# Kernel tuning notes

Hardware: AMD Instinct MI355X
Metric: run time of the kernel (lower is better)

## Reference

```python
import jax, jax.numpy as jnp
import numpy as np
import math

B, T, C, NH = 4, 2048, 1024, 16
D = C // NH  # 64, rotary_dim == D

def _rope_tables():
    inv_freq = 1.0 / (10000.0 ** (np.arange(0, D, 2, dtype=np.float32) / D))
    t = np.arange(T, dtype=np.float32)
    freqs = np.outer(t, inv_freq)                 # [T, D/2]
    emb = np.concatenate([freqs, freqs], axis=-1)  # [T, D]
    return jnp.asarray(np.cos(emb))[None], jnp.asarray(np.sin(emb))[None]  # [1,T,D]

def setup_inputs() -> dict:
    key = jax.random.key(0)
    ks = jax.random.split(key, 3)
    x = jax.random.normal(ks[0], (B, T, C), dtype=jnp.float32)
    w_attn = jax.random.normal(ks[1], (3 * C, C), dtype=jnp.float32) * (1.0 / math.sqrt(C))
    b_attn = jnp.zeros((3 * C,), dtype=jnp.float32)
    w_proj = jax.random.normal(ks[2], (C, C), dtype=jnp.float32) * (1.0 / math.sqrt(C))
    b_proj = jnp.zeros((C,), dtype=jnp.float32)
    cos, sin = _rope_tables()
    return {"x": x, "w_attn": w_attn, "b_attn": b_attn,
            "w_proj": w_proj, "b_proj": b_proj, "cos": cos, "sin": sin}

def _rotate_half(u):
    u1, u2 = jnp.split(u, 2, axis=-1)
    return jnp.concatenate([-u2, u1], axis=-1)

def reference(x, w_attn, b_attn, w_proj, b_proj, cos, sin):
    Bx, Tx, Cx = x.shape
    nh, d = NH, Cx // NH
    # fused QKV projection (torch Linear: y = x @ W^T + b)
    qkv = x @ w_attn.T + b_attn                      # [B,T,3C]
    q, k, v = jnp.split(qkv, 3, axis=-1)
    q = q.reshape(Bx, Tx, nh, d).transpose(0, 2, 1, 3)  # [B,nh,T,d]
    k = k.reshape(Bx, Tx, nh, d).transpose(0, 2, 1, 3)
    v = v.reshape(Bx, Tx, nh, d).transpose(0, 2, 1, 3)
    # RoPE (rotary_dim == d, full head)
    c = cos[:, None, :, :]  # [1,1,T,d]
    s = sin[:, None, :, :]
    q = q * c + _rotate_half(q) * s
    k = k * c + _rotate_half(k) * s
    # naive causal attention
    scores = jnp.einsum("bhqd,bhkd->bhqk", q, k) / math.sqrt(d)
    causal = jnp.tril(jnp.ones((Tx, Tx), dtype=bool))
    scores = jnp.where(causal[None, None], scores, -jnp.inf)
    att = jax.nn.softmax(scores, axis=-1)
    y = jnp.einsum("bhqk,bhkd->bhqd", att, v)        # [B,nh,T,d]
    y = y.transpose(0, 2, 1, 3).reshape(Bx, Tx, Cx)
    return y @ w_proj.T + b_proj
```

## Files before the change

### kernel.cpp

```cpp
#include <hip/hip_runtime.h>

typedef __bf16 bf16_t;
typedef bf16_t bf16x8 __attribute__((ext_vector_type(8)));
typedef bf16_t bf16x4 __attribute__((ext_vector_type(4)));
typedef float f32x4 __attribute__((ext_vector_type(4)));

constexpr int BATCH = 4, SEQ = 2048, CH = 1024, NHEAD = 16, HD = 64;
constexpr int BM = 128, BN = 128, BKK = 64;

#define LGKM_FENCE() __asm__ __volatile__("s_waitcnt lgkmcnt(0)" ::: "memory")
#define VM_FENCE() __asm__ __volatile__("s_waitcnt vmcnt(0)" ::: "memory")

__device__ __forceinline__ void g2lds16(const bf16_t* g, bf16_t* l) {
  __builtin_amdgcn_global_load_lds((__attribute__((address_space(1))) void*)(g),
                                   (__attribute__((address_space(3))) void*)(l),
                                   16, 0, 0);
}

__device__ __forceinline__ f32x4 mfma16(bf16x8 a, bf16x8 b, f32x4 c) {
  return __builtin_amdgcn_mfma_f32_16x16x32_bf16(a, b, c, 0, 0, 0);
}

__global__ __launch_bounds__(256) void cvt3_kernel(const float4* __restrict__ x,
                                                   ushort4* __restrict__ dx,
                                                   const float4* __restrict__ wa,
                                                   ushort4* __restrict__ dwa,
                                                   const float4* __restrict__ wp,
                                                   ushort4* __restrict__ dwp) {
  int bid = blockIdx.x;
  const float4* s;
  ushort4* d;
  int i;
  if (bid < 8192) {
    s = x; d = dx; i = bid * 256 + threadIdx.x;
  } else if (bid < 11264) {
    s = wa; d = dwa; i = (bid - 8192) * 256 + threadIdx.x;
  } else {
    s = wp; d = dwp; i = (bid - 11264) * 256 + threadIdx.x;
  }
  float4 f = s[i];
  ushort4 o;
  o.x = __builtin_bit_cast(unsigned short, (bf16_t)f.x);
  o.y = __builtin_bit_cast(unsigned short, (bf16_t)f.y);
  o.z = __builtin_bit_cast(unsigned short, (bf16_t)f.z);
  o.w = __builtin_bit_cast(unsigned short, (bf16_t)f.w);
  d[i] = o;
}

__device__ __forceinline__ void gemm_mainloop(const bf16_t* __restrict__ A,
                                              const bf16_t* __restrict__ W, int Kdim,
                                              int m0, int n0,
                                              bf16_t* As, bf16_t* Bs,
                                              f32x4 acc[4][4]) {
  const int tid = threadIdx.x;
  const int lane = tid & 63;
  const int w = tid >> 6;
  const int quad = lane >> 4, l16 = lane & 15;
  const int wm = (w >> 1) << 6, wn = (w & 1) << 6;
  const int srow = tid >> 3;
  const int scol = ((tid & 7) ^ (srow & 7)) << 3;
  const int dcol = (tid & 7) << 3;
  const int key = l16 & 15 & 7;
  const bf16_t* ga[4];
  const bf16_t* gb[4];
  bf16_t *la[4], *lb[4];
#pragma unroll
  for (int p = 0; p < 4; p++) {
    int row = p * 32 + srow;
    ga[p] = A + (size_t)(m0 + row) * Kdim + scol;
    gb[p] = W + (size_t)(n0 + row) * Kdim + scol;
    la[p] = As + row * BKK + dcol;
    lb[p] = Bs + row * BKK + dcol;
  }
  for (int k0 = 0; k0 < Kdim; k0 += BKK) {
#pragma unroll
    for (int p = 0; p < 4; p++) g2lds16(ga[p] + k0, la[p]);
#pragma unroll
    for (int p = 0; p < 4; p++) g2lds16(gb[p] + k0, lb[p]);
    VM_FENCE();
    __syncthreads();
#pragma unroll
    for (int ki = 0; ki < 2; ki++) {
      bf16x8 av[4], bv[4];
#pragma unroll
      for (int i = 0; i < 4; i++)
        av[i] = *(const bf16x8*)&As[(wm + i * 16 + l16) * BKK +
                                    ((((ki << 2) | quad) ^ key) << 3)];
#pragma unroll
      for (int i = 0; i < 4; i++)
        bv[i] = *(const bf16x8*)&Bs[(wn + i * 16 + l16) * BKK +
                                    ((((ki << 2) | quad) ^ key) << 3)];
#pragma unroll
      for (int mi = 0; mi < 4; mi++)
#pragma unroll
        for (int ni = 0; ni < 4; ni++)
          acc[mi][ni] = mfma16(av[mi], bv[ni], acc[mi][ni]);
    }
    __syncthreads();
  }
}

constexpr float SCL = 0.125f * 1.44269504089f;

__global__ __launch_bounds__(256) void qkv_rope_kernel(
    const bf16_t* __restrict__ X, const bf16_t* __restrict__ Wa,
    const float* __restrict__ ba, const float* __restrict__ cosT,
    const float* __restrict__ sinT, bf16_t* __restrict__ Q,
    bf16_t* __restrict__ Ko, bf16_t* __restrict__ VT) {
  constexpr int TSTRIDE = 68;
  __shared__ __align__(16) char smem[4 * 64 * TSTRIDE * 2];
  bf16_t* As = (bf16_t*)smem;
  bf16_t* Bs = As + BM * BKK;

  f32x4 acc[4][4];
#pragma unroll
  for (int i = 0; i < 4; i++)
#pragma unroll
    for (int j = 0; j < 4; j++) acc[i][j] = (f32x4){0.f, 0.f, 0.f, 0.f};

  const int id = blockIdx.x;
  const int sid = ((id & 7) * 192) + (id >> 3);
  const int n0 = (sid % 24) * BN;
  const int m0 = (sid / 24) * BM;
  gemm_mainloop(X, Wa, CH, m0, n0, As, Bs, acc);

  const int tid = threadIdx.x, lane = tid & 63, w = tid >> 6;
  const int quad = lane >> 4, l16 = lane & 15;
  const int wm = (w >> 1) << 6, wn = (w & 1) << 6;
  const int nbase = n0 + wn;
  const int part = nbase >> 10;
  const int h = (nbase & 1023) >> 6;
  const int mbase = m0 + wm;
  const int bb = mbase >> 11;
  const size_t headbase = ((size_t)(bb * NHEAD + h)) * SEQ * HD;

  if (part < 2) {
    bf16_t* O = (part == 0) ? Q : Ko;
    const float post = (part == 0) ? SCL : 1.0f;
#pragma unroll
    for (int mi = 0; mi < 4; mi++)
#pragma unroll
      for (int r = 0; r < 4; r++) {
        int m = mbase + mi * 16 + quad * 4 + r;
        int t = m & (SEQ - 1);
        const float* cr = cosT + t * HD;
        const float* sr = sinT + t * HD;
        size_t rowo = headbase + (size_t)t * HD;
#pragma unroll
        for (int ni = 0; ni < 2; ni++) {
          int d0 = ni * 16 + l16, d1 = d0 + 32;
          float v0 = acc[mi][ni][r] + ba[nbase + d0];
          float v1 = acc[mi][ni + 2][r] + ba[nbase + d1];
          float r0 = (v0 * cr[d0] - v1 * sr[d0]) * post;
          float r1 = (v1 * cr[d1] + v0 * sr[d1]) * post;
          O[rowo + d0] = (bf16_t)r0;
          O[rowo + d1] = (bf16_t)r1;
        }
      }
  } else {
    bf16_t* tb = (bf16_t*)smem + w * 64 * TSTRIDE;
    int t0 = mbase & (SEQ - 1);
#pragma unroll
    for (int mi = 0; mi < 4; mi++)
#pragma unroll
      for (int ni = 0; ni < 4; ni++) {
        int d = ni * 16 + l16;
        float bias = ba[nbase + d];
#pragma unroll
        for (int r = 0; r < 4; r++) {
          float v = acc[mi][ni][r] + bias;
          tb[d * TSTRIDE + mi * 16 + quad * 4 + r] = (bf16_t)v;
        }
      }
    LGKM_FENCE();
    int half = lane >> 5, l5 = lane & 31;
    size_t vbase = ((size_t)(bb * NHEAD + h)) * HD * SEQ;
#pragma unroll
    for (int it = 0; it < 32; it++) {
      int d = it * 2 + half;
      unsigned int val = *(const unsigned int*)&tb[d * TSTRIDE + l5 * 2];
      *(unsigned int*)&VT[vbase + (size_t)d * SEQ + t0 + l5 * 2] = val;
    }
  }
}

__device__ __forceinline__ void sm_update(f32x4 (&s)[4], float& lr,
                                          bf16_t* Prow, int quad,
                                          int swz, bool domask, int lim) {
  if (domask) {
#pragma unroll
    for (int ni = 0; ni < 4; ni++)
#pragma unroll
      for (int r = 0; r < 4; r++)
        if (ni * 16 + r > lim) s[ni][r] = -1e30f;
  }
  float sum = 0.f;
#pragma unroll
  for (int ni = 0; ni < 4; ni++) {
    float p0 = __builtin_exp2f(s[ni][0]);
    float p1 = __builtin_exp2f(s[ni][1]);
    float p2 = __builtin_exp2f(s[ni][2]);
    float p3 = __builtin_exp2f(s[ni][3]);
    bf16x4 pk = {(bf16_t)p0, (bf16_t)p1, (bf16_t)p2, (bf16_t)p3};
    *(bf16x4*)&Prow[(((ni << 2) | quad) ^ (swz << 1)) << 2] = pk;
    sum += (p0 + p1) + (p2 + p3);
  }
  lr += sum;
}

__global__ __launch_bounds__(256) void flash_kernel(const bf16_t* __restrict__ Q,
                                                    const bf16_t* __restrict__ Kg,
                                                    const bf16_t* __restrict__ VT,
                                                    bf16_t* __restrict__ att) {
  __shared__ __align__(16) bf16_t Ks[2][64 * 64];
  __shared__ __align__(16) bf16_t Vs[2][64 * 64];
  __shared__ __align__(16) bf16_t Pt[4][16 * 64];
  const int tid = threadIdx.x, w = tid >> 6, lane = tid & 63;
  const int quad = lane >> 4, l16 = lane & 15;
  const int p = (int)blockIdx.x >> 6;
  const int bh = (int)blockIdx.x & 63;
  const bf16_t* Qp = Q + (size_t)bh * SEQ * HD;
  const bf16_t* Kb = Kg + (size_t)bh * SEQ * HD;
  const bf16_t* Vb = VT + (size_t)bh * HD * SEQ;
  const int grow = lane >> 3;
  const int gj8 = ((lane & 7) ^ grow) * 8;
  const int i0 = w * 2;
  const int sw = l16 & 7;
  const int swz = l16 >> 1;
  const int bloc = bh >> 4, hh = bh & 15;
  bf16_t* Pw = &Pt[w][l16 * 64];
  const int rs0 = (quad ^ swz) << 3;
  const int rs1 = ((4 + quad) ^ swz) << 3;

  auto stage = [&](int kcs, int b) {
#pragma unroll
    for (int ii = 0; ii < 2; ii++) {
      int i = i0 + ii;
      g2lds16(Kb + (size_t)(kcs + i * 8 + grow) * HD + gj8, &Ks[b][(i * 64 + lane) * 8]);
      g2lds16(Vb + (size_t)(i * 8 + grow) * SEQ + kcs + gj8, &Vs[b][(i * 64 + lane) * 8]);
    }
  };

  for (int sp = 0; sp < 2; ++sp) {
    const int j = sp ? p : 31 - p;
    const int m = j * 64 + w * 16;
    const int nch = j + 1;
    bf16x8 aq0 = *(const bf16x8*)&Qp[(size_t)(m + l16) * HD + quad * 8];
    bf16x8 aq1 = *(const bf16x8*)&Qp[(size_t)(m + l16) * HD + 32 + quad * 8];
    float lr = 0.f;
    f32x4 y[4];
#pragma unroll
    for (int ni = 0; ni < 4; ni++) y[ni] = (f32x4){0.f, 0.f, 0.f, 0.f};

    stage(0, 0);
    VM_FENCE();
    __syncthreads();

    for (int c = 0; c < nch; ++c) {
      const int kc = c * 64, buf = c & 1;
      if (c + 1 < nch) stage(kc + 64, buf ^ 1);
      f32x4 s[4];
#pragma unroll
      for (int ni = 0; ni < 4; ni++) {
        bf16x8 k0 = *(const bf16x8*)&Ks[buf][((ni * 16 + l16) * 8 + (quad ^ sw)) * 8];
        bf16x8 k1 = *(const bf16x8*)&Ks[buf][((ni * 16 + l16) * 8 + ((4 + quad) ^ sw)) * 8];
        f32x4 z = (f32x4){0.f, 0.f, 0.f, 0.f};
        s[ni] = mfma16(k1, aq1, mfma16(k0, aq0, z));
      }
      sm_update(s, lr, Pw, quad, swz, c == nch - 1, m + l16 - kc - quad * 4);
      LGKM_FENCE();
      bf16x8 p0 = *(const bf16x8*)&Pw[rs0];
      bf16x8 p1 = *(const bf16x8*)&Pw[rs1];
#pragma unroll
      for (int ni = 0; ni < 4; ni++) {
        bf16x8 v0 = *(const bf16x8*)&Vs[buf][((ni * 16 + l16) * 8 + (quad ^ sw)) * 8];
        bf16x8 v1 = *(const bf16x8*)&Vs[buf][((ni * 16 + l16) * 8 + ((4 + quad) ^ sw)) * 8];
        y[ni] = mfma16(v1, p1, mfma16(v0, p0, y[ni]));
      }
      VM_FENCE();
      __syncthreads();
    }

    lr += __shfl_xor(lr, 16);
    lr += __shfl_xor(lr, 32);
    float inv = 1.f / lr;
    size_t rb = ((size_t)bloc * SEQ + m + l16) * CH + hh * HD + quad * 4;
#pragma unroll
    for (int ni = 0; ni < 4; ni++) {
      bf16x4 o = {(bf16_t)(y[ni][0] * inv), (bf16_t)(y[ni][1] * inv),
                  (bf16_t)(y[ni][2] * inv), (bf16_t)(y[ni][3] * inv)};
      *(bf16x4*)&att[rb + ni * 16] = o;
    }
  }
}

__global__ __launch_bounds__(256) void proj_kernel(const bf16_t* __restrict__ A,
                                                   const bf16_t* __restrict__ Wp,
                                                   const float* __restrict__ bp,
                                                   float* __restrict__ out) {
  __shared__ __align__(16) bf16_t As[BM * BKK];
  __shared__ __align__(16) bf16_t Bs[BN * BKK];
  f32x4 acc[4][4];
#pragma unroll
  for (int i = 0; i < 4; i++)
#pragma unroll
    for (int j = 0; j < 4; j++) acc[i][j] = (f32x4){0.f, 0.f, 0.f, 0.f};
  const int id = blockIdx.x;
  const int sid = ((id & 7) * 64) + (id >> 3);
  const int n0 = (sid % 8) * BN;
  const int m0 = (sid / 8) * BM;
  gemm_mainloop(A, Wp, CH, m0, n0, As, Bs, acc);
  const int tid = threadIdx.x, lane = tid & 63, w = tid >> 6;
  const int quad = lane >> 4, l16 = lane & 15;
  const int wm = (w >> 1) << 6, wn = (w & 1) << 6;
  const int nbase = n0 + wn, mbase = m0 + wm;
#pragma unroll
  for (int mi = 0; mi < 4; mi++)
#pragma unroll
    for (int r = 0; r < 4; r++) {
      int m = mbase + mi * 16 + quad * 4 + r;
#pragma unroll
      for (int ni = 0; ni < 4; ni++) {
        int n = nbase + ni * 16 + l16;
        out[(size_t)m * CH + n] = acc[mi][ni][r] + bp[n];
      }
    }
}

extern "C" void kernel_launch(void* const* d_in, const int* in_sizes, int n_in,
                              void* d_out, int out_size, void* d_ws, size_t ws_size,
                              hipStream_t stream) {
  const float* x      = (const float*)d_in[0];
  const float* w_attn = (const float*)d_in[1];
  const float* b_attn = (const float*)d_in[2];
  const float* w_proj = (const float*)d_in[3];
  const float* b_proj = (const float*)d_in[4];
  const float* cosT   = (const float*)d_in[5];
  const float* sinT   = (const float*)d_in[6];
  float* out = (float*)d_out;

  bf16_t* xbf  = (bf16_t*)d_ws;
  bf16_t* wabf = xbf + (size_t)8192 * 1024;
  bf16_t* wpbf = wabf + (size_t)3072 * 1024;
  bf16_t* Qb   = wpbf + (size_t)1024 * 1024;
  bf16_t* Kb   = Qb + (size_t)8388608;
  bf16_t* VTb  = Kb + (size_t)8388608;
  bf16_t* attb = VTb + (size_t)8388608;

  cvt3_kernel<<<12288, 256, 0, stream>>>((const float4*)x, (ushort4*)xbf,
                                         (const float4*)w_attn, (ushort4*)wabf,
                                         (const float4*)w_proj, (ushort4*)wpbf);
  qkv_rope_kernel<<<dim3(1536), 256, 0, stream>>>(xbf, wabf, b_attn, cosT, sinT,
                                                  Qb, Kb, VTb);
  flash_kernel<<<dim3(1024), 256, 0, stream>>>(Qb, Kb, VTb, attb);
  proj_kernel<<<dim3(512), 256, 0, stream>>>(attb, wpbf, b_proj, out);
}
```

Measured before the change: 266.8 us.

## Process two 64-row query tiles per warp group to reuse staged K/V chunks

Each flash attention block now handles a 128-row query block by giving every wave two 16-row query tiles, so each staged K/V chunk in LDS feeds twice as many MFMAs. The grid is halved to 512 blocks, with the two query tiles paired causally (15-p and p) to balance load. The P scratch buffer is doubled per wave. The cost is higher register pressure and fewer blocks in flight, which may reduce occupancy and hide latency less well.

After: 267.4 us. Within noise of the previous version (+0.2%).

```diff
diff --git a/kernel.cpp b/kernel.cpp
--- a/kernel.cpp
+++ b/kernel.cpp
@@ -60,7 +60,7 @@
   const int srow = tid >> 3;
   const int scol = ((tid & 7) ^ (srow & 7)) << 3;
   const int dcol = (tid & 7) << 3;
-  const int key = l16 & 15 & 7;
+  const int key = l16 & 7;
   const bf16_t* ga[4];
   const bf16_t* gb[4];
   bf16_t *la[4], *lb[4];
@@ -214,7 +214,7 @@
                                                     bf16_t* __restrict__ att) {
   __shared__ __align__(16) bf16_t Ks[2][64 * 64];
   __shared__ __align__(16) bf16_t Vs[2][64 * 64];
-  __shared__ __align__(16) bf16_t Pt[4][16 * 64];
+  __shared__ __align__(16) bf16_t Pt[4][2][16 * 64];
   const int tid = threadIdx.x, w = tid >> 6, lane = tid & 63;
   const int quad = lane >> 4, l16 = lane & 15;
   const int p = (int)blockIdx.x >> 6;
@@ -228,7 +228,8 @@
   const int sw = l16 & 7;
   const int swz = l16 >> 1;
   const int bloc = bh >> 4, hh = bh & 15;
-  bf16_t* Pw = &Pt[w][l16 * 64];
+  bf16_t* Pw0 = &Pt[w][0][l16 * 64];
+  bf16_t* Pw1 = &Pt[w][1][l16 * 64];
   const int rs0 = (quad ^ swz) << 3;
   const int rs1 = ((4 + quad) ^ swz) << 3;
 
@@ -242,15 +243,22 @@
   };
 
   for (int sp = 0; sp < 2; ++sp) {
-    const int j = sp ? p : 31 - p;
-    const int m = j * 64 + w * 16;
-    const int nch = j + 1;
-    bf16x8 aq0 = *(const bf16x8*)&Qp[(size_t)(m + l16) * HD + quad * 8];
-    bf16x8 aq1 = *(const bf16x8*)&Qp[(size_t)(m + l16) * HD + 32 + quad * 8];
-    float lr = 0.f;
-    f32x4 y[4];
-#pragma unroll
-    for (int ni = 0; ni < 4; ni++) y[ni] = (f32x4){0.f, 0.f, 0.f, 0.f};
+    const int jb = sp ? p : 15 - p;
+    const int mb = jb * 128;
+    const int m0t = mb + w * 16;
+    const int m1t = mb + 64 + w * 16;
+    const int nch = 2 * jb + 2;
+    bf16x8 aq00 = *(const bf16x8*)&Qp[(size_t)(m0t + l16) * HD + quad * 8];
+    bf16x8 aq01 = *(const bf16x8*)&Qp[(size_t)(m0t + l16) * HD + 32 + quad * 8];
+    bf16x8 aq10 = *(const bf16x8*)&Qp[(size_t)(m1t + l16) * HD + quad * 8];
+    bf16x8 aq11 = *(const bf16x8*)&Qp[(size_t)(m1t + l16) * HD + 32 + quad * 8];
+    float lr0 = 0.f, lr1 = 0.f;
+    f32x4 y0[4], y1[4];
+#pragma unroll
+    for (int ni = 0; ni < 4; ni++) {
+      y0[ni] = (f32x4){0.f, 0.f, 0.f, 0.f};
+      y1[ni] = (f32x4){0.f, 0.f, 0.f, 0.f};
+    }
 
     stage(0, 0);
     VM_FENCE();
@@ -259,37 +267,63 @@
     for (int c = 0; c < nch; ++c) {
       const int kc = c * 64, buf = c & 1;
       if (c + 1 < nch) stage(kc + 64, buf ^ 1);
-      f32x4 s[4];
-#pragma unroll
-      for (int ni = 0; ni < 4; ni++) {
-        bf16x8 k0 = *(const bf16x8*)&Ks[buf][((ni * 16 + l16) * 8 + (quad ^ sw)) * 8];
-        bf16x8 k1 = *(const bf16x8*)&Ks[buf][((ni * 16 + l16) * 8 + ((4 + quad) ^ sw)) * 8];
+      const bool do0 = (c + 1 < nch);
+      bf16x8 kf[8];
+#pragma unroll
+      for (int ni = 0; ni < 4; ni++) {
+        kf[2 * ni]     = *(const bf16x8*)&Ks[buf][((ni * 16 + l16) * 8 + (quad ^ sw)) * 8];
+        kf[2 * ni + 1] = *(const bf16x8*)&Ks[buf][((ni * 16 + l16) * 8 + ((4 + quad) ^ sw)) * 8];
+      }
+      f32x4 s0[4], s1[4];
+#pragma unroll
+      for (int ni = 0; ni < 4; ni++) {
         f32x4 z = (f32x4){0.f, 0.f, 0.f, 0.f};
-        s[ni] = mfma16(k1, aq1, mfma16(k0, aq0, z));
-      }
-      sm_update(s, lr, Pw, quad, swz, c == nch - 1, m + l16 - kc - quad * 4);
+        s1[ni] = mfma16(kf[2 * ni + 1], aq11, mfma16(kf[2 * ni], aq10, z));
+      }
+      if (do0) {
+#pragma unroll
+        for (int ni = 0; ni < 4; ni++) {
+          f32x4 z = (f32x4){0.f, 0.f, 0.f, 0.f};
+          s0[ni] = mfma16(kf[2 * ni + 1], aq01, mfma16(kf[2 * ni], aq00, z));
+        }
+      }
+      sm_update(s1, lr1, Pw1, quad, swz, c == nch - 1, m1t + l16 - kc - quad * 4);
+      if (do0)
+        sm_update(s0, lr0, Pw0, quad, swz, c == nch - 2, m0t + l16 - kc - quad * 4);
       LGKM_FENCE();
-      bf16x8 p0 = *(const bf16x8*)&Pw[rs0];
-      bf16x8 p1 = *(const bf16x8*)&Pw[rs1];
+      bf16x8 p10 = *(const bf16x8*)&Pw1[rs0];
+      bf16x8 p11 = *(const bf16x8*)&Pw1[rs1];
+      bf16x8 p00, p01;
+      if (do0) {
+        p00 = *(const bf16x8*)&Pw0[rs0];
+        p01 = *(const bf16x8*)&Pw0[rs1];
+      }
 #pragma unroll
       for (int ni = 0; ni < 4; ni++) {
         bf16x8 v0 = *(const bf16x8*)&Vs[buf][((ni * 16 + l16) * 8 + (quad ^ sw)) * 8];
         bf16x8 v1 = *(const bf16x8*)&Vs[buf][((ni * 16 + l16) * 8 + ((4 + quad) ^ sw)) * 8];
-        y[ni] = mfma16(v1, p1, mfma16(v0, p0, y[ni]));
+        y1[ni] = mfma16(v1, p11, mfma16(v0, p10, y1[ni]));
+        if (do0) y0[ni] = mfma16(v1, p01, mfma16(v0, p00, y0[ni]));
       }
       VM_FENCE();
       __syncthreads();
     }
 
-    lr += __shfl_xor(lr, 16);
-    lr += __shfl_xor(lr, 32);
-    float inv = 1.f / lr;
-    size_t rb = ((size_t)bloc * SEQ + m + l16) * CH + hh * HD + quad * 4;
+    lr0 += __shfl_xor(lr0, 16);
+    lr0 += __shfl_xor(lr0, 32);
+    lr1 += __shfl_xor(lr1, 16);
+    lr1 += __shfl_xor(lr1, 32);
+    float inv0 = 1.f / lr0, inv1 = 1.f / lr1;
+    size_t rb0 = ((size_t)bloc * SEQ + m0t + l16) * CH + hh * HD + quad * 4;
+    size_t rb1 = ((size_t)bloc * SEQ + m1t + l16) * CH + hh * HD + quad * 4;
 #pragma unroll
     for (int ni = 0; ni < 4; ni++) {
-      bf16x4 o = {(bf16_t)(y[ni][0] * inv), (bf16_t)(y[ni][1] * inv),
-                  (bf16_t)(y[ni][2] * inv), (bf16_t)(y[ni][3] * inv)};
-      *(bf16x4*)&att[rb + ni * 16] = o;
+      bf16x4 o0 = {(bf16_t)(y0[ni][0] * inv0), (bf16_t)(y0[ni][1] * inv0),
+                   (bf16_t)(y0[ni][2] * inv0), (bf16_t)(y0[ni][3] * inv0)};
+      bf16x4 o1 = {(bf16_t)(y1[ni][0] * inv1), (bf16_t)(y1[ni][1] * inv1),
+                   (bf16_t)(y1[ni][2] * inv1), (bf16_t)(y1[ni][3] * inv1)};
+      *(bf16x4*)&att[rb0 + ni * 16] = o0;
+      *(bf16x4*)&att[rb1 + ni * 16] = o1;
     }
   }
 }
@@ -352,6 +386,6 @@
                                          (const float4*)w_proj, (ushort4*)wpbf);
   qkv_rope_kernel<<<dim3(1536), 256, 0, stream>>>(xbf, wabf, b_attn, cosT, sinT,
                                                   Qb, Kb, VTb);
-  flash_kernel<<<dim3(1024), 256, 0, stream>>>(Qb, Kb, VTb, attb);
+  flash_kernel<<<dim3(512), 256, 0, stream>>>(Qb, Kb, VTb, attb);
   proj_kernel<<<dim3(512), 256, 0, stream>>>(attb, wpbf, b_proj, out);
 }
```

## Process paired high/low query tiles in one KV sweep sharing staged K/V

Applied to the files above, without the earlier changes.

Instead of two sequential passes (one for the high query tile, one for the low), the attention block streams K/V once and applies each chunk to both query tiles, with the low tile active only for its first chunks. This removes the second staging pass over K/V for the low tile and shares K fragments loaded from LDS between the two tiles. It also adds s_setprio around the MFMA sections to favour matrix issue. The cost is higher register pressure from two accumulator sets and extra Q fragments. The Pw scratch buffer is reused serially by both tiles within an iteration.

Measured after the change: 274.0 us. 1.03x slower.

```diff
diff --git a/kernel.cpp b/kernel.cpp
--- a/kernel.cpp
+++ b/kernel.cpp
@@ -60,7 +60,7 @@
   const int srow = tid >> 3;
   const int scol = ((tid & 7) ^ (srow & 7)) << 3;
   const int dcol = (tid & 7) << 3;
-  const int key = l16 & 15 & 7;
+  const int key = l16 & 7;
   const bf16_t* ga[4];
   const bf16_t* gb[4];
   bf16_t *la[4], *lb[4];
@@ -241,56 +241,100 @@
     }
   };
 
-  for (int sp = 0; sp < 2; ++sp) {
-    const int j = sp ? p : 31 - p;
-    const int m = j * 64 + w * 16;
-    const int nch = j + 1;
-    bf16x8 aq0 = *(const bf16x8*)&Qp[(size_t)(m + l16) * HD + quad * 8];
-    bf16x8 aq1 = *(const bf16x8*)&Qp[(size_t)(m + l16) * HD + 32 + quad * 8];
-    float lr = 0.f;
-    f32x4 y[4];
-#pragma unroll
-    for (int ni = 0; ni < 4; ni++) y[ni] = (f32x4){0.f, 0.f, 0.f, 0.f};
-
-    stage(0, 0);
-    VM_FENCE();
-    __syncthreads();
-
-    for (int c = 0; c < nch; ++c) {
-      const int kc = c * 64, buf = c & 1;
-      if (c + 1 < nch) stage(kc + 64, buf ^ 1);
+  const int jh = 31 - p, jl = p;
+  const int mh = jh * 64 + w * 16;
+  const int ml = jl * 64 + w * 16;
+  const int nch_h = 32 - p;
+  const int nch_l = p + 1;
+
+  bf16x8 aqh0 = *(const bf16x8*)&Qp[(size_t)(mh + l16) * HD + quad * 8];
+  bf16x8 aqh1 = *(const bf16x8*)&Qp[(size_t)(mh + l16) * HD + 32 + quad * 8];
+  bf16x8 aql0 = *(const bf16x8*)&Qp[(size_t)(ml + l16) * HD + quad * 8];
+  bf16x8 aql1 = *(const bf16x8*)&Qp[(size_t)(ml + l16) * HD + 32 + quad * 8];
+  float lrh = 0.f, lrl = 0.f;
+  f32x4 yh[4], yl[4];
+#pragma unroll
+  for (int ni = 0; ni < 4; ni++) {
+    yh[ni] = (f32x4){0.f, 0.f, 0.f, 0.f};
+    yl[ni] = (f32x4){0.f, 0.f, 0.f, 0.f};
+  }
+
+  stage(0, 0);
+  VM_FENCE();
+  __syncthreads();
+
+  for (int c = 0; c < nch_h; ++c) {
+    const int kc = c * 64, buf = c & 1;
+    if (c + 1 < nch_h) stage(kc + 64, buf ^ 1);
+    bf16x8 kf[8];
+#pragma unroll
+    for (int ni = 0; ni < 4; ni++) {
+      kf[2 * ni]     = *(const bf16x8*)&Ks[buf][((ni * 16 + l16) * 8 + (quad ^ sw)) * 8];
+      kf[2 * ni + 1] = *(const bf16x8*)&Ks[buf][((ni * 16 + l16) * 8 + ((4 + quad) ^ sw)) * 8];
+    }
+    {
       f32x4 s[4];
-#pragma unroll
-      for (int ni = 0; ni < 4; ni++) {
-        bf16x8 k0 = *(const bf16x8*)&Ks[buf][((ni * 16 + l16) * 8 + (quad ^ sw)) * 8];
-        bf16x8 k1 = *(const bf16x8*)&Ks[buf][((ni * 16 + l16) * 8 + ((4 + quad) ^ sw)) * 8];
+      __builtin_amdgcn_s_setprio(1);
+#pragma unroll
+      for (int ni = 0; ni < 4; ni++) {
         f32x4 z = (f32x4){0.f, 0.f, 0.f, 0.f};
-        s[ni] = mfma16(k1, aq1, mfma16(k0, aq0, z));
-      }
-      sm_update(s, lr, Pw, quad, swz, c == nch - 1, m + l16 - kc - quad * 4);
+        s[ni] = mfma16(kf[2 * ni + 1], aqh1, mfma16(kf[2 * ni], aqh0, z));
+      }
+      __builtin_amdgcn_s_setprio(0);
+      sm_update(s, lrh, Pw, quad, swz, c == nch_h - 1, mh + l16 - kc - quad * 4);
       LGKM_FENCE();
       bf16x8 p0 = *(const bf16x8*)&Pw[rs0];
       bf16x8 p1 = *(const bf16x8*)&Pw[rs1];
+      __builtin_amdgcn_s_setprio(1);
 #pragma unroll
       for (int ni = 0; ni < 4; ni++) {
         bf16x8 v0 = *(const bf16x8*)&Vs[buf][((ni * 16 + l16) * 8 + (quad ^ sw)) * 8];
         bf16x8 v1 = *(const bf16x8*)&Vs[buf][((ni * 16 + l16) * 8 + ((4 + quad) ^ sw)) * 8];
-        y[ni] = mfma16(v1, p1, mfma16(v0, p0, y[ni]));
-      }
-      VM_FENCE();
-      __syncthreads();
-    }
-
-    lr += __shfl_xor(lr, 16);
-    lr += __shfl_xor(lr, 32);
-    float inv = 1.f / lr;
-    size_t rb = ((size_t)bloc * SEQ + m + l16) * CH + hh * HD + quad * 4;
-#pragma unroll
-    for (int ni = 0; ni < 4; ni++) {
-      bf16x4 o = {(bf16_t)(y[ni][0] * inv), (bf16_t)(y[ni][1] * inv),
-                  (bf16_t)(y[ni][2] * inv), (bf16_t)(y[ni][3] * inv)};
-      *(bf16x4*)&att[rb + ni * 16] = o;
-    }
+        yh[ni] = mfma16(v1, p1, mfma16(v0, p0, yh[ni]));
+      }
+      __builtin_amdgcn_s_setprio(0);
+    }
+    if (c < nch_l) {
+      f32x4 s[4];
+      __builtin_amdgcn_s_setprio(1);
+#pragma unroll
+      for (int ni = 0; ni < 4; ni++) {
+        f32x4 z = (f32x4){0.f, 0.f, 0.f, 0.f};
+        s[ni] = mfma16(kf[2 * ni + 1], aql1, mfma16(kf[2 * ni], aql0, z));
+      }
+      __builtin_amdgcn_s_setprio(0);
+      sm_update(s, lrl, Pw, quad, swz, c == nch_l - 1, ml + l16 - kc - quad * 4);
+      LGKM_FENCE();
+      bf16x8 p0 = *(const bf16x8*)&Pw[rs0];
+      bf16x8 p1 = *(const bf16x8*)&Pw[rs1];
+      __builtin_amdgcn_s_setprio(1);
+#pragma unroll
+      for (int ni = 0; ni < 4; ni++) {
+        bf16x8 v0 = *(const bf16x8*)&Vs[buf][((ni * 16 + l16) * 8 + (quad ^ sw)) * 8];
+        bf16x8 v1 = *(const bf16x8*)&Vs[buf][((ni * 16 + l16) * 8 + ((4 + quad) ^ sw)) * 8];
+        yl[ni] = mfma16(v1, p1, mfma16(v0, p0, yl[ni]));
+      }
+      __builtin_amdgcn_s_setprio(0);
+    }
+    VM_FENCE();
+    __syncthreads();
+  }
+
+  lrh += __shfl_xor(lrh, 16);
+  lrh += __shfl_xor(lrh, 32);
+  lrl += __shfl_xor(lrl, 16);
+  lrl += __shfl_xor(lrl, 32);
+  float invh = 1.f / lrh, invl = 1.f / lrl;
+  size_t rbh = ((size_t)bloc * SEQ + mh + l16) * CH + hh * HD + quad * 4;
+  size_t rbl = ((size_t)bloc * SEQ + ml + l16) * CH + hh * HD + quad * 4;
+#pragma unroll
+  for (int ni = 0; ni < 4; ni++) {
+    bf16x4 oh = {(bf16_t)(yh[ni][0] * invh), (bf16_t)(yh[ni][1] * invh),
+                 (bf16_t)(yh[ni][2] * invh), (bf16_t)(yh[ni][3] * invh)};
+    bf16x4 ol = {(bf16_t)(yl[ni][0] * invl), (bf16_t)(yl[ni][1] * invl),
+                 (bf16_t)(yl[ni][2] * invl), (bf16_t)(yl[ni][3] * invl)};
+    *(bf16x4*)&att[rbh + ni * 16] = oh;
+    *(bf16x4*)&att[rbl + ni * 16] = ol;
   }
 }
 
```

## Double-buffer GEMM mainloop, shrink proj tile, compute softmax row sums via MFMA

Applied to the files above, without the earlier changes.

Replaces the single-buffered BK=64 GEMM mainloop with a templated double-buffered BK=32 loop that prefetches the next K slice while computing the current one, using partial vmcnt waits. This hides global-load latency in the QKV and projection GEMMs. The projection kernel switches to 64x128 tiles so its grid doubles to 1024 blocks for better occupancy. In flash attention the per-lane exp sums and cross-lane shuffles are replaced by an MFMA against a ones vector, which moves the row-sum work onto the matrix units at the cost of extra MFMA issue.

Result: slower. 277.0 us (+3.8%).

```diff
diff --git a/kernel.cpp b/kernel.cpp
--- a/kernel.cpp
+++ b/kernel.cpp
@@ -6,7 +6,7 @@
 typedef float f32x4 __attribute__((ext_vector_type(4)));
 
 constexpr int BATCH = 4, SEQ = 2048, CH = 1024, NHEAD = 16, HD = 64;
-constexpr int BM = 128, BN = 128, BKK = 64;
+constexpr int BM = 128, BN = 128;
 
 #define LGKM_FENCE() __asm__ __volatile__("s_waitcnt lgkmcnt(0)" ::: "memory")
 #define VM_FENCE() __asm__ __volatile__("s_waitcnt vmcnt(0)" ::: "memory")
@@ -47,55 +47,68 @@
   d[i] = o;
 }
 
-__device__ __forceinline__ void gemm_mainloop(const bf16_t* __restrict__ A,
-                                              const bf16_t* __restrict__ W, int Kdim,
-                                              int m0, int n0,
-                                              bf16_t* As, bf16_t* Bs,
-                                              f32x4 acc[4][4]) {
-  const int tid = threadIdx.x;
-  const int lane = tid & 63;
-  const int w = tid >> 6;
+template <int MFRAG, int NFRAG>
+__device__ __forceinline__ void gemm_db(const bf16_t* __restrict__ A,
+                                        const bf16_t* __restrict__ W,
+                                        int Kdim, int m0, int n0,
+                                        bf16_t* lds, f32x4 acc[MFRAG][NFRAG]) {
+  constexpr int MR = MFRAG * 32, NR = NFRAG * 32;
+  constexpr int AP = MR / 64, BP = NR / 64;
+  constexpr int ASZ = MR * 32, BSZ = NR * 32, BUF = ASZ + BSZ;
+  const int tid = threadIdx.x, lane = tid & 63, w = tid >> 6;
   const int quad = lane >> 4, l16 = lane & 15;
-  const int wm = (w >> 1) << 6, wn = (w & 1) << 6;
-  const int srow = tid >> 3;
-  const int scol = ((tid & 7) ^ (srow & 7)) << 3;
-  const int dcol = (tid & 7) << 3;
-  const int key = l16 & 15 & 7;
-  const bf16_t* ga[4];
-  const bf16_t* gb[4];
-  bf16_t *la[4], *lb[4];
-#pragma unroll
-  for (int p = 0; p < 4; p++) {
-    int row = p * 32 + srow;
-    ga[p] = A + (size_t)(m0 + row) * Kdim + scol;
-    gb[p] = W + (size_t)(n0 + row) * Kdim + scol;
-    la[p] = As + row * BKK + dcol;
-    lb[p] = Bs + row * BKK + dcol;
-  }
-  for (int k0 = 0; k0 < Kdim; k0 += BKK) {
-#pragma unroll
-    for (int p = 0; p < 4; p++) g2lds16(ga[p] + k0, la[p]);
-#pragma unroll
-    for (int p = 0; p < 4; p++) g2lds16(gb[p] + k0, lb[p]);
-    VM_FENCE();
+  const int wm = (w >> 1) * (MFRAG * 16), wn = (w & 1) * (NFRAG * 16);
+  const int srow = tid >> 2;
+  const int scol = (((tid & 3) ^ ((tid >> 3) & 3)) << 3);
+  const int dbase = srow * 32 + ((tid & 3) << 3);
+  const int key = (l16 >> 1) & 3;
+  const bf16_t* gA[AP];
+  const bf16_t* gB[BP];
+#pragma unroll
+  for (int p = 0; p < AP; p++)
+    gA[p] = A + (size_t)(m0 + p * 64 + srow) * Kdim + scol;
+#pragma unroll
+  for (int p = 0; p < BP; p++)
+    gB[p] = W + (size_t)(n0 + p * 64 + srow) * Kdim + scol;
+
+  auto stage = [&](int b, int k0) {
+#pragma unroll
+    for (int p = 0; p < AP; p++)
+      g2lds16(gA[p] + k0, lds + b * BUF + p * 2048 + dbase);
+#pragma unroll
+    for (int p = 0; p < BP; p++)
+      g2lds16(gB[p] + k0, lds + b * BUF + ASZ + p * 2048 + dbase);
+  };
+
+  stage(0, 0);
+  const int NIT = Kdim >> 5;
+  for (int t = 0; t < NIT; t++) {
+    const int b = t & 1;
+    if (t + 1 < NIT) stage(b ^ 1, (t + 1) << 5);
+    __builtin_amdgcn_sched_barrier(0);
+    if (t + 1 < NIT) {
+      if constexpr (AP + BP == 4)
+        asm volatile("s_waitcnt vmcnt(4)" ::: "memory");
+      else
+        asm volatile("s_waitcnt vmcnt(3)" ::: "memory");
+    } else {
+      VM_FENCE();
+    }
     __syncthreads();
-#pragma unroll
-    for (int ki = 0; ki < 2; ki++) {
-      bf16x8 av[4], bv[4];
-#pragma unroll
-      for (int i = 0; i < 4; i++)
-        av[i] = *(const bf16x8*)&As[(wm + i * 16 + l16) * BKK +
-                                    ((((ki << 2) | quad) ^ key) << 3)];
-#pragma unroll
-      for (int i = 0; i < 4; i++)
-        bv[i] = *(const bf16x8*)&Bs[(wn + i * 16 + l16) * BKK +
-                                    ((((ki << 2) | quad) ^ key) << 3)];
-#pragma unroll
-      for (int mi = 0; mi < 4; mi++)
-#pragma unroll
-        for (int ni = 0; ni < 4; ni++)
-          acc[mi][ni] = mfma16(av[mi], bv[ni], acc[mi][ni]);
-    }
+    const bf16_t* Ab = lds + b * BUF;
+    const bf16_t* Bb = Ab + ASZ;
+    bf16x8 av[MFRAG], bv[NFRAG];
+#pragma unroll
+    for (int i = 0; i < MFRAG; i++)
+      av[i] = *(const bf16x8*)&Ab[(wm + i * 16 + l16) * 32 + ((quad ^ key) << 3)];
+#pragma unroll
+    for (int i = 0; i < NFRAG; i++)
+      bv[i] = *(const bf16x8*)&Bb[(wn + i * 16 + l16) * 32 + ((quad ^ key) << 3)];
+#pragma unroll
+    for (int mi = 0; mi < MFRAG; mi++)
+#pragma unroll
+      for (int ni = 0; ni < NFRAG; ni++)
+        acc[mi][ni] = mfma16(av[mi], bv[ni], acc[mi][ni]);
     __syncthreads();
   }
 }
@@ -109,8 +122,6 @@
     bf16_t* __restrict__ Ko, bf16_t* __restrict__ VT) {
   constexpr int TSTRIDE = 68;
   __shared__ __align__(16) char smem[4 * 64 * TSTRIDE * 2];
-  bf16_t* As = (bf16_t*)smem;
-  bf16_t* Bs = As + BM * BKK;
 
   f32x4 acc[4][4];
 #pragma unroll
@@ -122,7 +133,7 @@
   const int sid = ((id & 7) * 192) + (id >> 3);
   const int n0 = (sid % 24) * BN;
   const int m0 = (sid / 24) * BM;
-  gemm_mainloop(X, Wa, CH, m0, n0, As, Bs, acc);
+  gemm_db<4, 4>(X, Wa, CH, m0, n0, (bf16_t*)smem, acc);
 
   const int tid = threadIdx.x, lane = tid & 63, w = tid >> 6;
   const int quad = lane >> 4, l16 = lane & 15;
@@ -184,8 +195,7 @@
   }
 }
 
-__device__ __forceinline__ void sm_update(f32x4 (&s)[4], float& lr,
-                                          bf16_t* Prow, int quad,
+__device__ __forceinline__ void sm_update(f32x4 (&s)[4], bf16_t* Prow, int quad,
                                           int swz, bool domask, int lim) {
   if (domask) {
 #pragma unroll
@@ -194,7 +204,6 @@
       for (int r = 0; r < 4; r++)
         if (ni * 16 + r > lim) s[ni][r] = -1e30f;
   }
-  float sum = 0.f;
 #pragma unroll
   for (int ni = 0; ni < 4; ni++) {
     float p0 = __builtin_exp2f(s[ni][0]);
@@ -203,9 +212,7 @@
     float p3 = __builtin_exp2f(s[ni][3]);
     bf16x4 pk = {(bf16_t)p0, (bf16_t)p1, (bf16_t)p2, (bf16_t)p3};
     *(bf16x4*)&Prow[(((ni << 2) | quad) ^ (swz << 1)) << 2] = pk;
-    sum += (p0 + p1) + (p2 + p3);
-  }
-  lr += sum;
+  }
 }
 
 __global__ __launch_bounds__(256) void flash_kernel(const bf16_t* __restrict__ Q,
@@ -232,6 +239,9 @@
   const int rs0 = (quad ^ swz) << 3;
   const int rs1 = ((4 + quad) ^ swz) << 3;
 
+  const bf16x8 ones = {(bf16_t)1.f, (bf16_t)1.f, (bf16_t)1.f, (bf16_t)1.f,
+                       (bf16_t)1.f, (bf16_t)1.f, (bf16_t)1.f, (bf16_t)1.f};
+
   auto stage = [&](int kcs, int b) {
 #pragma unroll
     for (int ii = 0; ii < 2; ii++) {
@@ -247,8 +257,8 @@
     const int nch = j + 1;
     bf16x8 aq0 = *(const bf16x8*)&Qp[(size_t)(m + l16) * HD + quad * 8];
     bf16x8 aq1 = *(const bf16x8*)&Qp[(size_t)(m + l16) * HD + 32 + quad * 8];
-    float lr = 0.f;
     f32x4 y[4];
+    f32x4 sum_acc = (f32x4){0.f, 0.f, 0.f, 0.f};
 #pragma unroll
     for (int ni = 0; ni < 4; ni++) y[ni] = (f32x4){0.f, 0.f, 0.f, 0.f};
 
@@ -267,10 +277,11 @@
         f32x4 z = (f32x4){0.f, 0.f, 0.f, 0.f};
         s[ni] = mfma16(k1, aq1, mfma16(k0, aq0, z));
       }
-      sm_update(s, lr, Pw, quad, swz, c == nch - 1, m + l16 - kc - quad * 4);
+      sm_update(s, Pw, quad, swz, c == nch - 1, m + l16 - kc - quad * 4);
       LGKM_FENCE();
       bf16x8 p0 = *(const bf16x8*)&Pw[rs0];
       bf16x8 p1 = *(const bf16x8*)&Pw[rs1];
+      sum_acc = mfma16(ones, p1, mfma16(ones, p0, sum_acc));
 #pragma unroll
       for (int ni = 0; ni < 4; ni++) {
         bf16x8 v0 = *(const bf16x8*)&Vs[buf][((ni * 16 + l16) * 8 + (quad ^ sw)) * 8];
@@ -281,9 +292,7 @@
       __syncthreads();
     }
 
-    lr += __shfl_xor(lr, 16);
-    lr += __shfl_xor(lr, 32);
-    float inv = 1.f / lr;
+    float inv = 1.f / sum_acc[0];
     size_t rb = ((size_t)bloc * SEQ + m + l16) * CH + hh * HD + quad * 4;
 #pragma unroll
     for (int ni = 0; ni < 4; ni++) {
@@ -298,24 +307,25 @@
                                                    const bf16_t* __restrict__ Wp,
                                                    const float* __restrict__ bp,
                                                    float* __restrict__ out) {
-  __shared__ __align__(16) bf16_t As[BM * BKK];
-  __shared__ __align__(16) bf16_t Bs[BN * BKK];
-  f32x4 acc[4][4];
-#pragma unroll
-  for (int i = 0; i < 4; i++)
+  __shared__ __align__(16) bf16_t lds[2 * (64 * 32 + 128 * 32)];
+  f32x4 acc[2][4];
+#pragma unroll
+  for (int i = 0; i < 2; i++)
 #pragma unroll
     for (int j = 0; j < 4; j++) acc[i][j] = (f32x4){0.f, 0.f, 0.f, 0.f};
+
   const int id = blockIdx.x;
-  const int sid = ((id & 7) * 64) + (id >> 3);
-  const int n0 = (sid % 8) * BN;
-  const int m0 = (sid / 8) * BM;
-  gemm_mainloop(A, Wp, CH, m0, n0, As, Bs, acc);
+  const int sid = ((id & 7) * 128) + (id >> 3);
+  const int n0 = (sid % 8) * 128;
+  const int m0 = (sid / 8) * 64;
+  gemm_db<2, 4>(A, Wp, CH, m0, n0, lds, acc);
+
   const int tid = threadIdx.x, lane = tid & 63, w = tid >> 6;
   const int quad = lane >> 4, l16 = lane & 15;
-  const int wm = (w >> 1) << 6, wn = (w & 1) << 6;
+  const int wm = (w >> 1) << 5, wn = (w & 1) << 6;
   const int nbase = n0 + wn, mbase = m0 + wm;
 #pragma unroll
-  for (int mi = 0; mi < 4; mi++)
+  for (int mi = 0; mi < 2; mi++)
 #pragma unroll
     for (int r = 0; r < 4; r++) {
       int m = mbase + mi * 16 + quad * 4 + r;
@@ -353,5 +363,5 @@
   qkv_rope_kernel<<<dim3(1536), 256, 0, stream>>>(xbf, wabf, b_attn, cosT, sinT,
                                                   Qb, Kb, VTb);
   flash_kernel<<<dim3(1024), 256, 0, stream>>>(Qb, Kb, VTb, attb);
-  proj_kernel<<<dim3(512), 256, 0, stream>>>(attb, wpbf, b_proj, out);
-}
+  proj_kernel<<<dim3(1024), 256, 0, stream>>>(attb, wpbf, b_proj, out);
+}
```
